# Kernel optimization log

Measured on AMD Instinct MI355X. Metric: run time of the kernel, lower is better.

The kernel has to match this reference:

```python
import jax, jax.numpy as jnp
import numpy as np

NUM_NODES = 102400
NUM_EDGES = 3276800
NUM_GRAPHS = 1024
LAMBDA_MAX = 2.0


def setup_inputs() -> dict:
    key = jax.random.key(0)
    ks = jax.random.split(key, 12)
    inp = {}
    inp['x'] = jax.random.normal(ks[0], (NUM_NODES, 128), dtype=jnp.float32)
    inp['edge_index'] = jax.random.randint(ks[1], (2, NUM_EDGES), 0, NUM_NODES, dtype=jnp.int32).astype(jnp.int64)
    inp['edge_attr'] = jax.random.uniform(ks[2], (NUM_EDGES,), dtype=jnp.float32)
    inp['batch'] = jnp.sort(jax.random.randint(ks[3], (NUM_NODES,), 0, NUM_GRAPHS, dtype=jnp.int32).astype(jnp.int64))
    inp['w1'] = jax.random.normal(ks[4], (3, 128, 64), dtype=jnp.float32) * 0.05
    inp['b1'] = jax.random.normal(ks[5], (64,), dtype=jnp.float32) * 0.05
    inp['w2'] = jax.random.normal(ks[6], (3, 64, 64), dtype=jnp.float32) * 0.05
    inp['b2'] = jax.random.normal(ks[7], (64,), dtype=jnp.float32) * 0.05
    inp['w3'] = jax.random.normal(ks[8], (3, 64, 128), dtype=jnp.float32) * 0.05
    inp['b3'] = jax.random.normal(ks[9], (128,), dtype=jnp.float32) * 0.05
    inp['lin_w'] = jax.random.normal(ks[10], (128, 2), dtype=jnp.float32) * 0.05
    inp['lin_b'] = jax.random.normal(ks[11], (2,), dtype=jnp.float32) * 0.05
    return inp


def _cheb_norm(edge_index, edge_attr, num_nodes):
    # PyG ChebConv.__norm__ with normalization='sym', lambda_max=2.0:
    #   L = I - D^{-1/2} A D^{-1/2};  Lhat = (2/lambda_max) * L - I
    # off-diagonal weights: -(2/lmax) * d_i^{-1/2} w_ij d_j^{-1/2}
    # diagonal coefficient:  (2/lmax) - 1  (== 0 for lmax = 2)
    src, dst = edge_index[0], edge_index[1]
    deg = jax.ops.segment_sum(edge_attr, src, num_segments=num_nodes)
    dinv = jnp.where(deg > 0, jax.lax.rsqrt(jnp.where(deg > 0, deg, 1.0)), 0.0)
    w = -(2.0 / LAMBDA_MAX) * dinv[src] * edge_attr * dinv[dst]
    diag = (2.0 / LAMBDA_MAX) - 1.0
    return w, diag


def _cheb_conv(x, src, dst, norm_w, diag, weight, bias):
    # weight: [K, Fin, Fout]; Chebyshev recurrence T0=x, T1=Lhat x, Tk=2 Lhat T_{k-1} - T_{k-2}
    n = x.shape[0]

    def spmv(v):  # Lhat @ v via edge-list scatter/gather
        return jax.ops.segment_sum(norm_w[:, None] * v[src], dst, num_segments=n) + diag * v

    Tx0 = x
    out = Tx0 @ weight[0]
    Tx1 = spmv(Tx0)
    out = out + Tx1 @ weight[1]
    for k in range(2, weight.shape[0]):
        Tx2 = 2.0 * spmv(Tx1) - Tx0
        out = out + Tx2 @ weight[k]
        Tx0, Tx1 = Tx1, Tx2
    return out + bias


def reference(x, edge_index, edge_attr, batch, w1, b1, w2, b2, w3, b3, lin_w, lin_b):
    n = x.shape[0]
    src, dst = edge_index[0], edge_index[1]
    norm_w, diag = _cheb_norm(edge_index, edge_attr, n)
    h = jax.nn.relu(_cheb_conv(x, src, dst, norm_w, diag, w1, b1))
    h = jax.nn.relu(_cheb_conv(h, src, dst, norm_w, diag, w2, b2))
    h = jax.nn.relu(_cheb_conv(h, src, dst, norm_w, diag, w3, b3))
    # global_mean_pool over graph ids
    sums = jax.ops.segment_sum(h, batch, num_segments=NUM_GRAPHS)
    cnts = jax.ops.segment_sum(jnp.ones((n,), h.dtype), batch, num_segments=NUM_GRAPHS)
    pooled = sums / jnp.maximum(cnts, 1.0)[:, None]
    return pooled @ lin_w + lin_b
```

## Files before the change

### kernel.cpp

```cpp
#include <hip/hip_runtime.h>
#include <cstddef>
#include <cstdint>

#define N_NODES 102400
#define N_EDGES 3276800
#define N_GRAPHS 1024
#define NBUCK 400
#define NBB 1024
#define EPB 3200
#define N64 ((size_t)N_NODES * 64)

typedef unsigned short ushortT;
typedef unsigned int uintT;
typedef __attribute__((ext_vector_type(8))) short bf16x8;
typedef __attribute__((ext_vector_type(4))) float f32x4;

__device__ __forceinline__ float b2f(ushortT h) {
    return __uint_as_float(((uintT)h) << 16);
}
__device__ __forceinline__ ushortT f2b(float f) {
    uintT u = __float_as_uint(f);
    uintT r = (u + 0x7fffu + ((u >> 16) & 1u)) >> 16;
    return (ushortT)r;
}
__device__ __forceinline__ float loF(uintT w) { return __uint_as_float(w << 16); }
__device__ __forceinline__ float hiF(uintT w) { return __uint_as_float(w & 0xffff0000u); }

__global__ __launch_bounds__(256) void k_binA(const int* __restrict__ src,
                                              const int* __restrict__ dst,
                                              int* __restrict__ blkCntD,
                                              int* __restrict__ blkCntS) {
    __shared__ int hd[NBUCK], hs[NBUCK];
    int t = threadIdx.x;
    for (int i = t; i < NBUCK; i += 256) { hd[i] = 0; hs[i] = 0; }
    __syncthreads();
    int base = blockIdx.x * EPB;
    const int4* s4 = (const int4*)(src + base);
    const int4* d4 = (const int4*)(dst + base);
    for (int v = t; v < EPB / 4; v += 256) {
        int4 d = d4[v];
        int4 s = s4[v];
        atomicAdd(&hd[d.x >> 8], 1);
        atomicAdd(&hd[d.y >> 8], 1);
        atomicAdd(&hd[d.z >> 8], 1);
        atomicAdd(&hd[d.w >> 8], 1);
        atomicAdd(&hs[s.x >> 8], 1);
        atomicAdd(&hs[s.y >> 8], 1);
        atomicAdd(&hs[s.z >> 8], 1);
        atomicAdd(&hs[s.w >> 8], 1);
    }
    __syncthreads();
    for (int i = t; i < NBUCK; i += 256) {
        blkCntD[(size_t)blockIdx.x * NBUCK + i] = hd[i];
        blkCntS[(size_t)blockIdx.x * NBUCK + i] = hs[i];
    }
}

__global__ void k_tr(const int* __restrict__ inD, const int* __restrict__ inS,
                     int* __restrict__ outD, int* __restrict__ outS) {
    __shared__ int tile[32][33];
    const int* in = blockIdx.z ? inS : inD;
    int* out = blockIdx.z ? outS : outD;
    int x = blockIdx.x * 32 + threadIdx.x;
    int yb = blockIdx.y * 32;
    for (int dy = threadIdx.y; dy < 32; dy += 8) {
        int y = yb + dy;
        tile[dy][threadIdx.x] = (x < NBUCK) ? in[(size_t)y * NBUCK + x] : 0;
    }
    __syncthreads();
    int xo = yb + threadIdx.x;
    for (int dy = threadIdx.y; dy < 32; dy += 8) {
        int bo = blockIdx.x * 32 + dy;
        if (bo < NBUCK) out[(size_t)bo * NBB + xo] = tile[threadIdx.x][dy];
    }
}

__global__ __launch_bounds__(512) void k_bbase(const int* __restrict__ blkCntT,
                                               int* __restrict__ blkRel,
                                               int* __restrict__ bucketTot) {
    __shared__ int sc[NBB];
    int b = blockIdx.x, t = threadIdx.x;
    int v0 = blkCntT[(size_t)b * NBB + t];
    int v1 = blkCntT[(size_t)b * NBB + t + 512];
    sc[t] = v0; sc[t + 512] = v1;
    __syncthreads();
    for (int o = 1; o < NBB; o <<= 1) {
        int x0 = (t >= o) ? sc[t - o] : 0;
        int x1 = (t + 512 >= o) ? sc[t + 512 - o] : 0;
        __syncthreads();
        sc[t] += x0; sc[t + 512] += x1;
        __syncthreads();
    }
    blkRel[(size_t)t * NBUCK + b] = sc[t] - v0;
    blkRel[(size_t)(t + 512) * NBUCK + b] = sc[t + 512] - v1;
    if (t == 511) bucketTot[b] = sc[NBB - 1];
}

__global__ __launch_bounds__(512) void k_bscan(const int* __restrict__ bucketTotD,
                                               const int* __restrict__ bucketTotS,
                                               int* __restrict__ binBaseD,
                                               int* __restrict__ binBaseS,
                                               int* __restrict__ rowp) {
    __shared__ int sc[512];
    int t = threadIdx.x;
    int vD = (t < NBUCK) ? bucketTotD[t] : 0;
    sc[t] = vD;
    __syncthreads();
    for (int o = 1; o < 512; o <<= 1) {
        int x = (t >= o) ? sc[t - o] : 0;
        __syncthreads();
        sc[t] += x;
        __syncthreads();
    }
    if (t < NBUCK) binBaseD[t] = sc[t] - vD;
    if (t == 511) { binBaseD[NBUCK] = sc[511]; rowp[N_NODES] = sc[511]; }
    __syncthreads();
    int vS = (t < NBUCK) ? bucketTotS[t] : 0;
    sc[t] = vS;
    __syncthreads();
    for (int o = 1; o < 512; o <<= 1) {
        int x = (t >= o) ? sc[t - o] : 0;
        __syncthreads();
        sc[t] += x;
        __syncthreads();
    }
    if (t < NBUCK) binBaseS[t] = sc[t] - vS;
    if (t == 511) binBaseS[NBUCK] = sc[511];
}

__global__ __launch_bounds__(512) void k_binB2(const int* __restrict__ src,
                                               const int* __restrict__ dst,
                                               const float* __restrict__ attr,
                                               const int* __restrict__ blkCntD,
                                               const int* __restrict__ blkCntS,
                                               const int* __restrict__ blkRelD,
                                               const int* __restrict__ blkRelS,
                                               const int* __restrict__ binBaseD,
                                               const int* __restrict__ binBaseS,
                                               int2* __restrict__ edsD,
                                               int2* __restrict__ edsS) {
    __shared__ int sxD[EPB];
    __shared__ int syD[EPB];
    __shared__ ushortT spD[EPB];
    __shared__ int sxS[EPB];
    __shared__ int syS[EPB];
    __shared__ ushortT spS[EPB];
    __shared__ int lcurD[NBUCK], deltaD[NBUCK];
    __shared__ int lcurS[NBUCK], deltaS[NBUCK];
    int bx = blockIdx.x, t = threadIdx.x;

    int vD = (t < NBUCK) ? blkCntD[(size_t)bx * NBUCK + t] : 0;
    int vS = (t < NBUCK) ? blkCntS[(size_t)bx * NBUCK + t] : 0;
    sxD[t] = vD; sxS[t] = vS;
    __syncthreads();
    for (int o = 1; o < 512; o <<= 1) {
        int xD = (t >= o) ? sxD[t - o] : 0;
        int xS = (t >= o) ? sxS[t - o] : 0;
        __syncthreads();
        sxD[t] += xD; sxS[t] += xS;
        __syncthreads();
    }
    if (t < NBUCK) {
        int eD = sxD[t] - vD;
        lcurD[t] = eD;
        deltaD[t] = binBaseD[t] + blkRelD[(size_t)bx * NBUCK + t] - eD;
        int eS = sxS[t] - vS;
        lcurS[t] = eS;
        deltaS[t] = binBaseS[t] + blkRelS[(size_t)bx * NBUCK + t] - eS;
    }
    __syncthreads();

    int base = bx * EPB;
    for (int v = t; v < EPB / 2; v += 512) {
        int e0 = base + v * 2;
        int2 s2 = *(const int2*)(src + e0);
        int2 d2 = *(const int2*)(dst + e0);
        float2 a2 = *(const float2*)(attr + e0);
        int bkt, lp;
        bkt = d2.x >> 8;
        lp = atomicAdd(&lcurD[bkt], 1);
        spD[lp] = (ushortT)bkt; sxD[lp] = (s2.x << 8) | (d2.x & 255);
        syD[lp] = __float_as_int(a2.x);
        bkt = s2.x >> 8;
        lp = atomicAdd(&lcurS[bkt], 1);
        spS[lp] = (ushortT)bkt; sxS[lp] = s2.x & 255;
        syS[lp] = __float_as_int(a2.x);
        bkt = d2.y >> 8;
        lp = atomicAdd(&lcurD[bkt], 1);
        spD[lp] = (ushortT)bkt; sxD[lp] = (s2.y << 8) | (d2.y & 255);
        syD[lp] = __float_as_int(a2.y);
        bkt = s2.y >> 8;
        lp = atomicAdd(&lcurS[bkt], 1);
        spS[lp] = (ushortT)bkt; sxS[lp] = s2.y & 255;
        syS[lp] = __float_as_int(a2.y);
    }
    __syncthreads();
    for (int i = t; i < EPB; i += 512) {
        edsD[i + deltaD[spD[i]]] = make_int2(sxD[i], syD[i]);
        edsS[i + deltaS[spS[i]]] = make_int2(sxS[i], syS[i]);
    }
}

__global__ __launch_bounds__(256) void k_deg(const int2* __restrict__ edsS,
                                             const int* __restrict__ binBaseS,
                                             float* __restrict__ dinv) {
    __shared__ float degL[256];
    int b = blockIdx.x, t = threadIdx.x;
    degL[t] = 0.f;
    __syncthreads();
    int s0 = binBaseS[b], s1 = binBaseS[b + 1];
    for (int i = s0 + t; i < s1; i += 256) {
        int2 e = edsS[i];
        atomicAdd(&degL[e.x], __int_as_float(e.y));
    }
    __syncthreads();
    float d = degL[t];
    dinv[b * 256 + t] = d > 0.f ? rsqrtf(d) : 0.f;
}

__global__ __launch_bounds__(512) void k_csr(const int2* __restrict__ edsD,
                                             const int* __restrict__ binBaseD,
                                             const float* __restrict__ dinvG,
                                             int* __restrict__ rowp,
                                             int2* __restrict__ cedge) {
    __shared__ int cntL[256];
    __shared__ int curL[256];
    __shared__ float dL[256];
    int b = blockIdx.x, t = threadIdx.x;
    if (t < 256) { cntL[t] = 0; dL[t] = dinvG[b * 256 + t]; }
    __syncthreads();
    int s0 = binBaseD[b], s1 = binBaseD[b + 1];
    for (int i = s0 + t; i < s1; i += 512) {
        atomicAdd(&cntL[edsD[i].x & 255], 1);
    }
    __syncthreads();
    int v = (t < 256) ? cntL[t] : 0;
    for (int o = 1; o < 256; o <<= 1) {
        int x = (t < 256 && t >= o) ? cntL[t - o] : 0;
        __syncthreads();
        if (t < 256) cntL[t] += x;
        __syncthreads();
    }
    if (t < 256) {
        int excl = cntL[t] - v;
        curL[t] = s0 + excl;
        rowp[b * 256 + t] = s0 + excl;
    }
    __syncthreads();
    for (int i = s0 + t; i < s1; i += 512) {
        int2 e = edsD[i];
        int dl = e.x & 255;
        int sg = e.x >> 8;
        float w = -__int_as_float(e.y) * dinvG[sg] * dL[dl];
        int p = atomicAdd(&curL[dl], 1);
        cedge[p] = make_int2(sg, __float_as_int(w));
    }
}

__global__ __launch_bounds__(256) void k_cast(const float* __restrict__ x,
                                              ushortT* __restrict__ Xhi,
                                              ushortT* __restrict__ Xlo) {
    int i = blockIdx.x * 256 + threadIdx.x;
    int n = i >> 5;
    int kq = (i & 31) * 4;
    float4 v = ((const float4*)x)[i];
    int s = kq >> 6, kk = kq & 63;
    size_t o = (size_t)s * N64 + (size_t)n * 64 + kk;
    ushort4 h, l;
    h.x = f2b(v.x); l.x = f2b(v.x - b2f(h.x));
    h.y = f2b(v.y); l.y = f2b(v.y - b2f(h.y));
    h.z = f2b(v.z); l.z = f2b(v.z - b2f(h.z));
    h.w = f2b(v.w); l.w = f2b(v.w - b2f(h.w));
    *(ushort4*)(Xhi + o) = h;
    *(ushort4*)(Xlo + o) = l;
}

__global__ void k_wprepAll(const float* __restrict__ w1f,
                           const float* __restrict__ w2f,
                           const float* __restrict__ w3f,
                           ushortT* __restrict__ Wt1h, ushortT* __restrict__ Wt1l,
                           ushortT* __restrict__ Wt2h, ushortT* __restrict__ Wt2l,
                           ushortT* __restrict__ Wt3h, ushortT* __restrict__ Wt3l) {
    int bid = blockIdx.x;
    float v;
    if (bid < 96) {
        int i = bid * 256 + threadIdx.x;
        int n = i / 128, k = i % 128;
        const float* w = w1f;
        if (n < 64)       v = w[k * 64 + n] - w[16384 + k * 64 + n];
        else if (n < 128) v = w[8192 + k * 64 + (n - 64)];
        else              v = w[16384 + k * 64 + (n - 128)];
        ushortT h = f2b(v);
        Wt1h[i] = h;
        Wt1l[i] = f2b(v - b2f(h));
    } else if (bid < 144) {
        int i = (bid - 96) * 256 + threadIdx.x;
        int n = i / 64, k = i % 64;
        const float* w = w2f;
        if (n < 64)       v = w[k * 64 + n] - w[8192 + k * 64 + n];
        else if (n < 128) v = w[4096 + k * 64 + (n - 64)];
        else              v = w[8192 + k * 64 + (n - 128)];
        ushortT h = f2b(v);
        Wt2h[i] = h;
        Wt2l[i] = f2b(v - b2f(h));
    } else {
        int i = (bid - 144) * 256 + threadIdx.x;
        int n = i / 192, k = i % 192;
        v = w3f[(k >> 6) * 8192 + (k & 63) * 128 + n];
        ushortT h = f2b(v);
        Wt3h[i] = h;
        Wt3l[i] = f2b(v - b2f(h));
    }
}

template <int KTOT, int NTOT, int MODE>
__global__ __launch_bounds__(512) void k_mgemm(
    const ushortT* __restrict__ Ah0, const ushortT* __restrict__ Ah1,
    const ushortT* __restrict__ Ah2, const ushortT* __restrict__ Al0,
    const ushortT* __restrict__ Al1, const ushortT* __restrict__ Al2,
    const ushortT* __restrict__ Wth, const ushortT* __restrict__ Wtl,
    const float* __restrict__ bias, float* __restrict__ outf,
    ushortT* __restrict__ outb, const int* __restrict__ batch,
    float* __restrict__ pooled, float* __restrict__ gcnt) {
    constexpr int KPAD = 72;
    constexpr int NCT = NTOT / 16;
    constexpr int SMEM_STAGE = 2 * NTOT * KPAD * 2;
    constexpr int SMEM_POOL = (MODE == 1) ? (256 * 128 * 4 + 256 * 4) : 0;
    constexpr int SMEM_BYTES = SMEM_STAGE > SMEM_POOL ? SMEM_STAGE : SMEM_POOL;
    __shared__ __align__(16) char smem[SMEM_BYTES];
    ushortT* Bh = (ushortT*)smem;
    ushortT* Bl = Bh + NTOT * KPAD;
    const ushortT* Ah[3] = {Ah0, Ah1, Ah2};
    const ushortT* Al[3] = {Al0, Al1, Al2};
    int t = threadIdx.x;
    int lane = t & 63;
    int wv = t >> 6;
    int m = lane & 15, q = lane >> 4;
    int r0 = blockIdx.x * 256 + wv * 32;
    int ar0 = r0 + m;
    int ar1 = r0 + 16 + m;

    f32x4 acc[2][NCT];
#pragma unroll
    for (int rf = 0; rf < 2; rf++)
#pragma unroll
        for (int ct = 0; ct < NCT; ct++)
#pragma unroll
            for (int j = 0; j < 4; j++) acc[rf][ct][j] = 0.f;

#pragma unroll
    for (int kc = 0; kc < KTOT / 64; kc++) {
        __syncthreads();
        for (int i = t; i < NTOT * 8; i += 512) {
            int col = i >> 3, k = (i & 7) * 8;
            *(uint4*)(Bh + col * KPAD + k) =
                *(const uint4*)(Wth + (size_t)col * KTOT + kc * 64 + k);
            *(uint4*)(Bl + col * KPAD + k) =
                *(const uint4*)(Wtl + (size_t)col * KTOT + kc * 64 + k);
        }
        __syncthreads();
        const ushortT* Ahc = Ah[kc];
        const ushortT* Alc = Al[kc];
#pragma unroll
        for (int ks2 = 0; ks2 < 2; ks2++) {
            int kk = ks2 * 32 + q * 8;
            bf16x8 ah0 = *(const bf16x8*)(Ahc + (size_t)ar0 * 64 + kk);
            bf16x8 al0 = *(const bf16x8*)(Alc + (size_t)ar0 * 64 + kk);
            bf16x8 ah1 = *(const bf16x8*)(Ahc + (size_t)ar1 * 64 + kk);
            bf16x8 al1 = *(const bf16x8*)(Alc + (size_t)ar1 * 64 + kk);
#pragma unroll
            for (int ct = 0; ct < NCT; ct++) {
                int bo = (ct * 16 + m) * KPAD + ks2 * 32 + q * 8;
                bf16x8 bh = *(const bf16x8*)(Bh + bo);
                bf16x8 bl = *(const bf16x8*)(Bl + bo);
                acc[0][ct] = __builtin_amdgcn_mfma_f32_16x16x32_bf16(ah0, bh, acc[0][ct], 0, 0, 0);
                acc[0][ct] = __builtin_amdgcn_mfma_f32_16x16x32_bf16(al0, bh, acc[0][ct], 0, 0, 0);
                acc[0][ct] = __builtin_amdgcn_mfma_f32_16x16x32_bf16(ah0, bl, acc[0][ct], 0, 0, 0);
                acc[1][ct] = __builtin_amdgcn_mfma_f32_16x16x32_bf16(ah1, bh, acc[1][ct], 0, 0, 0);
                acc[1][ct] = __builtin_amdgcn_mfma_f32_16x16x32_bf16(al1, bh, acc[1][ct], 0, 0, 0);
                acc[1][ct] = __builtin_amdgcn_mfma_f32_16x16x32_bf16(ah1, bl, acc[1][ct], 0, 0, 0);
            }
        }
    }

    if (MODE == 0) {
#pragma unroll
        for (int rf = 0; rf < 2; rf++)
#pragma unroll
            for (int ct = 0; ct < NCT; ct++)
#pragma unroll
                for (int rg = 0; rg < 4; rg++) {
                    int row = r0 + rf * 16 + q * 4 + rg;
                    float v = acc[rf][ct][rg];
                    if (ct < 8)
                        outf[(size_t)row * 128 + ct * 16 + m] = v;
                    else
                        outb[(size_t)row * 64 + (ct - 8) * 16 + m] = f2b(v);
                }
    } else {
        float* poolB = (float*)smem;
        int* batchL = (int*)(smem + 256 * 128 * 4);
        __syncthreads();
        for (int i = t; i < 256; i += 512)
            batchL[i] = batch[blockIdx.x * 256 + i];
#pragma unroll
        for (int rf = 0; rf < 2; rf++)
#pragma unroll
            for (int ct = 0; ct < NCT; ct++)
#pragma unroll
                for (int rg = 0; rg < 4; rg++) {
                    int rl = wv * 32 + rf * 16 + q * 4 + rg;
                    int col = ct * 16 + m;
                    poolB[rl * 128 + col] = fmaxf(acc[rf][ct][rg] + bias[col], 0.f);
                }
        __syncthreads();
        int col = t & 127, seg = t >> 7;
        int base = seg * 64;
        int g = batchL[base];
        float a = 0.f;
        int c = 0;
        for (int k = 0; k < 64; k++) {
            int gn = batchL[base + k];
            if (gn != g) {
                atomicAdd(&pooled[(size_t)g * 128 + col], a);
                if (col == 0) atomicAdd(&gcnt[g], (float)c);
                g = gn; a = 0.f; c = 0;
            }
            a += poolB[(base + k) * 128 + col];
            c++;
        }
        atomicAdd(&pooled[(size_t)g * 128 + col], a);
        if (col == 0) atomicAdd(&gcnt[g], (float)c);
    }
}

template <int MODE, int SA, bool AUXB, bool WLO>
__global__ __launch_bounds__(256) void k_spmm(const int* __restrict__ rowp,
                                              const int2* __restrict__ cedge,
                                              const ushortT* __restrict__ Xb,
                                              const float* __restrict__ auxF,
                                              const ushortT* __restrict__ auxH,
                                              const ushortT* __restrict__ auxL,
                                              const float* __restrict__ bias,
                                              ushortT* __restrict__ Yh,
                                              ushortT* __restrict__ Yl) {
    int node = blockIdx.x * 4 + (threadIdx.x >> 6);
    int lane = threadIdx.x & 63;
    int q = lane >> 3;
    int f = (lane & 7) * 8;
    int s = rowp[node], e = rowp[node + 1];
    const ushortT* Xf = Xb + f;
    float a0 = 0.f, a1 = 0.f, a2 = 0.f, a3 = 0.f;
    float a4 = 0.f, a5 = 0.f, a6 = 0.f, a7 = 0.f;
    for (int i = s; i < e; i += 16) {
        int i0 = min(i + q, e - 1);
        int i1 = min(i + 8 + q, e - 1);
        int2 ed0 = cedge[i0];
        int2 ed1 = cedge[i1];
        float w0 = (i + q < e) ? __int_as_float(ed0.y) : 0.f;
        float w1 = (i + 8 + q < e) ? __int_as_float(ed1.y) : 0.f;
        uint4 u0 = *(const uint4*)(Xf + ((size_t)ed0.x << 6));
        uint4 u1 = *(const uint4*)(Xf + ((size_t)ed1.x << 6));
        a0 = fmaf(w0, loF(u0.x), a0);
        a1 = fmaf(w0, hiF(u0.x), a1);
        a2 = fmaf(w0, loF(u0.y), a2);
        a3 = fmaf(w0, hiF(u0.y), a3);
        a4 = fmaf(w0, loF(u0.z), a4);
        a5 = fmaf(w0, hiF(u0.z), a5);
        a6 = fmaf(w0, loF(u0.w), a6);
        a7 = fmaf(w0, hiF(u0.w), a7);
        a0 = fmaf(w1, loF(u1.x), a0);
        a1 = fmaf(w1, hiF(u1.x), a1);
        a2 = fmaf(w1, loF(u1.y), a2);
        a3 = fmaf(w1, hiF(u1.y), a3);
        a4 = fmaf(w1, loF(u1.z), a4);
        a5 = fmaf(w1, hiF(u1.z), a5);
        a6 = fmaf(w1, loF(u1.w), a6);
        a7 = fmaf(w1, hiF(u1.w), a7);
    }
    a0 += __shfl_xor(a0, 8); a0 += __shfl_xor(a0, 16); a0 += __shfl_xor(a0, 32);
    a1 += __shfl_xor(a1, 8); a1 += __shfl_xor(a1, 16); a1 += __shfl_xor(a1, 32);
    a2 += __shfl_xor(a2, 8); a2 += __shfl_xor(a2, 16); a2 += __shfl_xor(a2, 32);
    a3 += __shfl_xor(a3, 8); a3 += __shfl_xor(a3, 16); a3 += __shfl_xor(a3, 32);
    a4 += __shfl_xor(a4, 8); a4 += __shfl_xor(a4, 16); a4 += __shfl_xor(a4, 32);
    a5 += __shfl_xor(a5, 8); a5 += __shfl_xor(a5, 16); a5 += __shfl_xor(a5, 32);
    a6 += __shfl_xor(a6, 8); a6 += __shfl_xor(a6, 16); a6 += __shfl_xor(a6, 32);
    a7 += __shfl_xor(a7, 8); a7 += __shfl_xor(a7, 16); a7 += __shfl_xor(a7, 32);

    if (q == 0 || (WLO && q == 1)) {
        float x0 = 0.f, x1 = 0.f, x2 = 0.f, x3 = 0.f;
        float x4 = 0.f, x5 = 0.f, x6 = 0.f, x7 = 0.f;
        if (MODE != 0) {
            if (AUXB) {
                uint4 ha = *(const uint4*)(auxH + (size_t)node * 64 + f);
                uint4 la = *(const uint4*)(auxL + (size_t)node * 64 + f);
                x0 = loF(ha.x) + loF(la.x);
                x1 = hiF(ha.x) + hiF(la.x);
                x2 = loF(ha.y) + loF(la.y);
                x3 = hiF(ha.y) + hiF(la.y);
                x4 = loF(ha.z) + loF(la.z);
                x5 = hiF(ha.z) + hiF(la.z);
                x6 = loF(ha.w) + loF(la.w);
                x7 = hiF(ha.w) + hiF(la.w);
            } else {
                float4 av0 = *(const float4*)(auxF + (size_t)node * SA + f);
                float4 av1 = *(const float4*)(auxF + (size_t)node * SA + f + 4);
                x0 = av0.x; x1 = av0.y; x2 = av0.z; x3 = av0.w;
                x4 = av1.x; x5 = av1.y; x6 = av1.z; x7 = av1.w;
            }
        }
        float r0, r1, r2, r3, r4, r5, r6, r7;
        if (MODE == 0) {
            r0 = a0; r1 = a1; r2 = a2; r3 = a3;
            r4 = a4; r5 = a5; r6 = a6; r7 = a7;
        } else if (MODE == 1) {
            r0 = x0 + 2.f * a0; r1 = x1 + 2.f * a1;
            r2 = x2 + 2.f * a2; r3 = x3 + 2.f * a3;
            r4 = x4 + 2.f * a4; r5 = x5 + 2.f * a5;
            r6 = x6 + 2.f * a6; r7 = x7 + 2.f * a7;
        } else if (MODE == 2) {
            r0 = 2.f * a0 - x0; r1 = 2.f * a1 - x1;
            r2 = 2.f * a2 - x2; r3 = 2.f * a3 - x3;
            r4 = 2.f * a4 - x4; r5 = 2.f * a5 - x5;
            r6 = 2.f * a6 - x6; r7 = 2.f * a7 - x7;
        } else {
            float4 bv0 = *(const float4*)(bias + f);
            float4 bv1 = *(const float4*)(bias + f + 4);
            r0 = fmaxf(x0 + a0 + bv0.x, 0.f);
            r1 = fmaxf(x1 + a1 + bv0.y, 0.f);
            r2 = fmaxf(x2 + a2 + bv0.z, 0.f);
            r3 = fmaxf(x3 + a3 + bv0.w, 0.f);
            r4 = fmaxf(x4 + a4 + bv1.x, 0.f);
            r5 = fmaxf(x5 + a5 + bv1.y, 0.f);
            r6 = fmaxf(x6 + a6 + bv1.z, 0.f);
            r7 = fmaxf(x7 + a7 + bv1.w, 0.f);
        }
        ushortT h0 = f2b(r0), h1 = f2b(r1), h2 = f2b(r2), h3 = f2b(r3);
        ushortT h4 = f2b(r4), h5 = f2b(r5), h6 = f2b(r6), h7 = f2b(r7);
        if (q == 0) {
            uint4 pk;
            pk.x = (uintT)h0 | ((uintT)h1 << 16);
            pk.y = (uintT)h2 | ((uintT)h3 << 16);
            pk.z = (uintT)h4 | ((uintT)h5 << 16);
            pk.w = (uintT)h6 | ((uintT)h7 << 16);
            *(uint4*)(Yh + (size_t)node * 64 + f) = pk;
        } else {
            uint4 pk;
            pk.x = (uintT)f2b(r0 - b2f(h0)) | ((uintT)f2b(r1 - b2f(h1)) << 16);
            pk.y = (uintT)f2b(r2 - b2f(h2)) | ((uintT)f2b(r3 - b2f(h3)) << 16);
            pk.z = (uintT)f2b(r4 - b2f(h4)) | ((uintT)f2b(r5 - b2f(h5)) << 16);
            pk.w = (uintT)f2b(r6 - b2f(h6)) | ((uintT)f2b(r7 - b2f(h7)) << 16);
            *(uint4*)(Yl + (size_t)node * 64 + f) = pk;
        }
    }
}

__global__ void k_final(const float* __restrict__ pooled, const float* __restrict__ gcnt,
                        const float* __restrict__ lin_w, const float* __restrict__ lin_b,
                        float* __restrict__ out) {
    int g = blockIdx.x * 4 + (threadIdx.x >> 6);
    int lane = threadIdx.x & 63;
    if (g >= N_GRAPHS) return;
    float inv = 1.f / fmaxf(gcnt[g], 1.f);
    float v0 = pooled[(size_t)g * 128 + lane] * inv;
    float v1 = pooled[(size_t)g * 128 + 64 + lane] * inv;
    float p0 = v0 * lin_w[lane * 2 + 0] + v1 * lin_w[(lane + 64) * 2 + 0];
    float p1 = v0 * lin_w[lane * 2 + 1] + v1 * lin_w[(lane + 64) * 2 + 1];
    for (int o = 32; o > 0; o >>= 1) {
        p0 += __shfl_down(p0, o);
        p1 += __shfl_down(p1, o);
    }
    if (lane == 0) {
        out[g * 2 + 0] = p0 + lin_b[0];
        out[g * 2 + 1] = p1 + lin_b[1];
    }
}

extern "C" void kernel_launch(void* const* d_in, const int* in_sizes, int n_in,
                              void* d_out, int out_size, void* d_ws, size_t ws_size,
                              hipStream_t stream) {
    const float* x     = (const float*)d_in[0];
    const int*   src   = (const int*)d_in[1];
    const int*   dst   = src + N_EDGES;
    const float* eattr = (const float*)d_in[2];
    const int*   batch = (const int*)d_in[3];
    const float* w1    = (const float*)d_in[4];
    const float* b1    = (const float*)d_in[5];
    const float* w2    = (const float*)d_in[6];
    const float* b2    = (const float*)d_in[7];
    const float* w3    = (const float*)d_in[8];
    const float* b3    = (const float*)d_in[9];
    const float* lin_w = (const float*)d_in[10];
    const float* lin_b = (const float*)d_in[11];
    float* out = (float*)d_out;

    char* ws = (char*)d_ws;
    size_t off = 0;
    auto alloc = [&](size_t bytes) -> char* {
        char* p = ws + off;
        off += (bytes + 255) & ~(size_t)255;
        return p;
    };
    int*   blkCntD   = (int*)  alloc((size_t)NBB * NBUCK * 4);
    int*   blkCntS   = (int*)  alloc((size_t)NBB * NBUCK * 4);
    int*   blkCntDT  = (int*)  alloc((size_t)NBUCK * NBB * 4);
    int*   blkCntST  = (int*)  alloc((size_t)NBUCK * NBB * 4);
    int*   blkRelD   = (int*)  alloc((size_t)NBB * NBUCK * 4);
    int*   blkRelS   = (int*)  alloc((size_t)NBB * NBUCK * 4);
    int*   bucketTotD = (int*) alloc(NBUCK * 4);
    int*   bucketTotS = (int*) alloc(NBUCK * 4);
    int*   binBaseD  = (int*)  alloc((NBUCK + 1) * 4);
    int*   binBaseS  = (int*)  alloc((NBUCK + 1) * 4);
    float* dinv      = (float*)alloc((size_t)N_NODES * 4);
    int*   rowp      = (int*)  alloc((size_t)(N_NODES + 1) * 4);
    ushortT* Wt1h   = (ushortT*)alloc(192 * 128 * 2);
    ushortT* Wt1l   = (ushortT*)alloc(192 * 128 * 2);
    ushortT* Wt2h   = (ushortT*)alloc(192 * 64 * 2);
    ushortT* Wt2l   = (ushortT*)alloc(192 * 64 * 2);
    ushortT* Wt3h   = (ushortT*)alloc(128 * 192 * 2);
    ushortT* Wt3l   = (ushortT*)alloc(128 * 192 * 2);
    float* pooled   = (float*)alloc((size_t)(N_GRAPHS * 128 + N_GRAPHS) * 4);
    float* gcnt     = pooled + (size_t)N_GRAPHS * 128;
    int2*  cedge    = (int2*) alloc((size_t)N_EDGES * 8);
    char*  Buf1     = alloc((size_t)N_EDGES * 16);
    char*  Buf2     = alloc((size_t)N_NODES * 128 * 4);
    char*  Buf3     = alloc(4 * N64 * 2);

    int2* edsD = (int2*)Buf1;
    int2* edsS = edsD + N_EDGES;
    ushortT* Xhi  = (ushortT*)Buf1;
    ushortT* Xlo  = Xhi + 2 * N64;
    ushortT* GThi = (ushortT*)Buf1;
    float* P  = (float*)Buf2;
    ushortT* G0    = (ushortT*)Buf3;
    ushortT* Qhi   = G0 + N64;
    ushortT* H1hi  = G0 + 2 * N64;
    ushortT* H1lo  = G0 + 3 * N64;
    ushortT* GTlo0 = G0;
    ushortT* GTlo1 = H1hi;
    ushortT* GTlo2 = H1lo;

    hipMemsetAsync(pooled, 0, (size_t)(N_GRAPHS * 128 + N_GRAPHS) * 4, stream);

    k_binA<<<NBB, 256, 0, stream>>>(src, dst, blkCntD, blkCntS);
    k_tr<<<dim3(13, 32, 2), dim3(32, 8), 0, stream>>>(blkCntD, blkCntS,
                                                      blkCntDT, blkCntST);
    k_bbase<<<NBUCK, 512, 0, stream>>>(blkCntDT, blkRelD, bucketTotD);
    k_bbase<<<NBUCK, 512, 0, stream>>>(blkCntST, blkRelS, bucketTotS);
    k_bscan<<<1, 512, 0, stream>>>(bucketTotD, bucketTotS, binBaseD, binBaseS, rowp);
    k_binB2<<<NBB, 512, 0, stream>>>(src, dst, eattr, blkCntD, blkCntS,
                                     blkRelD, blkRelS, binBaseD, binBaseS,
                                     edsD, edsS);
    k_deg<<<NBUCK, 256, 0, stream>>>(edsS, binBaseS, dinv);
    k_csr<<<NBUCK, 512, 0, stream>>>(edsD, binBaseD, dinv, rowp, cedge);

    k_cast<<<N_NODES * 32 / 256, 256, 0, stream>>>(x, Xhi, Xlo);
    k_wprepAll<<<240, 256, 0, stream>>>(w1, w2, w3, Wt1h, Wt1l, Wt2h, Wt2l,
                                        Wt3h, Wt3l);

    k_mgemm<128, 192, 0><<<N_NODES / 256, 512, 0, stream>>>(
        Xhi, Xhi + N64, nullptr, Xlo, Xlo + N64, nullptr, Wt1h, Wt1l, nullptr,
        P, G0, nullptr, nullptr, nullptr);
    k_spmm<1, 128, false, false><<<N_NODES / 4, 256, 0, stream>>>(
        rowp, cedge, G0, P + 64, nullptr, nullptr, nullptr, Qhi, nullptr);
    k_spmm<3, 128, false, true><<<N_NODES / 4, 256, 0, stream>>>(
        rowp, cedge, Qhi, P, nullptr, nullptr, b1, H1hi, H1lo);

    k_mgemm<64, 192, 0><<<N_NODES / 256, 512, 0, stream>>>(
        H1hi, nullptr, nullptr, H1lo, nullptr, nullptr, Wt2h, Wt2l, nullptr,
        P, G0, nullptr, nullptr, nullptr);
    k_spmm<1, 128, false, false><<<N_NODES / 4, 256, 0, stream>>>(
        rowp, cedge, G0, P + 64, nullptr, nullptr, nullptr, Qhi, nullptr);
    k_spmm<3, 128, false, true><<<N_NODES / 4, 256, 0, stream>>>(
        rowp, cedge, Qhi, P, nullptr, nullptr, b2, GThi, GTlo0);

    k_spmm<0, 64, false, true><<<N_NODES / 4, 256, 0, stream>>>(
        rowp, cedge, GThi, nullptr, nullptr, nullptr, nullptr, GThi + N64, GTlo1);
    k_spmm<2, 64, true, true><<<N_NODES / 4, 256, 0, stream>>>(
        rowp, cedge, GThi + N64, nullptr, GThi, GTlo0, nullptr, GThi + 2 * N64, GTlo2);
    k_mgemm<192, 128, 1><<<N_NODES / 256, 512, 0, stream>>>(
        GThi, GThi + N64, GThi + 2 * N64, GTlo0, GTlo1, GTlo2, Wt3h, Wt3l, b3,
        nullptr, nullptr, batch, pooled, gcnt);

    k_final<<<N_GRAPHS / 4, 256, 0, stream>>>(pooled, gcnt, lin_w, lin_b, out);
}
```

Before: 715.0 us.

## Halve binning block size and shrink GEMM LDS stage to 32-wide K chunks

The edge binning now uses 2048 blocks of 1600 edges instead of 1024 blocks of 3200. This shrinks per-block shared memory and spreads the work over more blocks, so the block-base scan now has each thread prefix four entries serially. The MFMA GEMM stages the weight tile in 32-wide K chunks with a smaller padded LDS buffer, cutting LDS use to allow more resident blocks. The cost is twice as many barrier-separated weight loads, and more count and offset arrays to scan.

```diff
diff --git a/kernel.cpp b/kernel.cpp
--- a/kernel.cpp
+++ b/kernel.cpp
@@ -6,8 +6,8 @@
 #define N_EDGES 3276800
 #define N_GRAPHS 1024
 #define NBUCK 400
-#define NBB 1024
-#define EPB 3200
+#define NBB 2048
+#define EPB 1600
 #define N64 ((size_t)N_NODES * 64)
 
 typedef unsigned short ushortT;
@@ -78,22 +78,30 @@
 __global__ __launch_bounds__(512) void k_bbase(const int* __restrict__ blkCntT,
                                                int* __restrict__ blkRel,
                                                int* __restrict__ bucketTot) {
-    __shared__ int sc[NBB];
+    __shared__ int sc[512];
     int b = blockIdx.x, t = threadIdx.x;
-    int v0 = blkCntT[(size_t)b * NBB + t];
-    int v1 = blkCntT[(size_t)b * NBB + t + 512];
-    sc[t] = v0; sc[t + 512] = v1;
-    __syncthreads();
-    for (int o = 1; o < NBB; o <<= 1) {
-        int x0 = (t >= o) ? sc[t - o] : 0;
-        int x1 = (t + 512 >= o) ? sc[t + 512 - o] : 0;
-        __syncthreads();
-        sc[t] += x0; sc[t + 512] += x1;
-        __syncthreads();
-    }
-    blkRel[(size_t)t * NBUCK + b] = sc[t] - v0;
-    blkRel[(size_t)(t + 512) * NBUCK + b] = sc[t + 512] - v1;
-    if (t == 511) bucketTot[b] = sc[NBB - 1];
+    int v[4];
+    int loc = 0;
+#pragma unroll
+    for (int j = 0; j < 4; j++) {
+        v[j] = blkCntT[(size_t)b * NBB + t * 4 + j];
+        loc += v[j];
+    }
+    sc[t] = loc;
+    __syncthreads();
+    for (int o = 1; o < 512; o <<= 1) {
+        int x = (t >= o) ? sc[t - o] : 0;
+        __syncthreads();
+        sc[t] += x;
+        __syncthreads();
+    }
+    int run = sc[t] - loc;
+#pragma unroll
+    for (int j = 0; j < 4; j++) {
+        blkRel[(size_t)(t * 4 + j) * NBUCK + b] = run;
+        run += v[j];
+    }
+    if (t == 511) bucketTot[b] = run;
 }
 
 __global__ __launch_bounds__(512) void k_bscan(const int* __restrict__ bucketTotD,
@@ -171,28 +179,20 @@
     __syncthreads();
 
     int base = bx * EPB;
-    for (int v = t; v < EPB / 2; v += 512) {
-        int e0 = base + v * 2;
-        int2 s2 = *(const int2*)(src + e0);
-        int2 d2 = *(const int2*)(dst + e0);
-        float2 a2 = *(const float2*)(attr + e0);
+    for (int v = t; v < EPB; v += 512) {
+        int e0 = base + v;
+        int s0 = src[e0];
+        int d0 = dst[e0];
+        float a0 = attr[e0];
         int bkt, lp;
-        bkt = d2.x >> 8;
+        bkt = d0 >> 8;
         lp = atomicAdd(&lcurD[bkt], 1);
-        spD[lp] = (ushortT)bkt; sxD[lp] = (s2.x << 8) | (d2.x & 255);
-        syD[lp] = __float_as_int(a2.x);
-        bkt = s2.x >> 8;
+        spD[lp] = (ushortT)bkt; sxD[lp] = (s0 << 8) | (d0 & 255);
+        syD[lp] = __float_as_int(a0);
+        bkt = s0 >> 8;
         lp = atomicAdd(&lcurS[bkt], 1);
-        spS[lp] = (ushortT)bkt; sxS[lp] = s2.x & 255;
-        syS[lp] = __float_as_int(a2.x);
-        bkt = d2.y >> 8;
-        lp = atomicAdd(&lcurD[bkt], 1);
-        spD[lp] = (ushortT)bkt; sxD[lp] = (s2.y << 8) | (d2.y & 255);
-        syD[lp] = __float_as_int(a2.y);
-        bkt = s2.y >> 8;
-        lp = atomicAdd(&lcurS[bkt], 1);
-        spS[lp] = (ushortT)bkt; sxS[lp] = s2.y & 255;
-        syS[lp] = __float_as_int(a2.y);
+        spS[lp] = (ushortT)bkt; sxS[lp] = s0 & 255;
+        syS[lp] = __float_as_int(a0);
     }
     __syncthreads();
     for (int i = t; i < EPB; i += 512) {
@@ -322,7 +322,7 @@
     const float* __restrict__ bias, float* __restrict__ outf,
     ushortT* __restrict__ outb, const int* __restrict__ batch,
     float* __restrict__ pooled, float* __restrict__ gcnt) {
-    constexpr int KPAD = 72;
+    constexpr int KPAD = 40;
     constexpr int NCT = NTOT / 16;
     constexpr int SMEM_STAGE = 2 * NTOT * KPAD * 2;
     constexpr int SMEM_POOL = (MODE == 1) ? (256 * 128 * 4 + 256 * 4) : 0;
@@ -349,37 +349,36 @@
             for (int j = 0; j < 4; j++) acc[rf][ct][j] = 0.f;
 
 #pragma unroll
-    for (int kc = 0; kc < KTOT / 64; kc++) {
-        __syncthreads();
-        for (int i = t; i < NTOT * 8; i += 512) {
-            int col = i >> 3, k = (i & 7) * 8;
+    for (int kc = 0; kc < KTOT / 32; kc++) {
+        __syncthreads();
+        for (int i = t; i < NTOT * 4; i += 512) {
+            int col = i >> 2, k = (i & 3) * 8;
             *(uint4*)(Bh + col * KPAD + k) =
-                *(const uint4*)(Wth + (size_t)col * KTOT + kc * 64 + k);
+                *(const uint4*)(Wth + (size_t)col * KTOT + kc * 32 + k);
             *(uint4*)(Bl + col * KPAD + k) =
-                *(const uint4*)(Wtl + (size_t)col * KTOT + kc * 64 + k);
+                *(const uint4*)(Wtl + (size_t)col * KTOT + kc * 32 + k);
         }
         __syncthreads();
-        const ushortT* Ahc = Ah[kc];
-        const ushortT* Alc = Al[kc];
-#pragma unroll
-        for (int ks2 = 0; ks2 < 2; ks2++) {
-            int kk = ks2 * 32 + q * 8;
-            bf16x8 ah0 = *(const bf16x8*)(Ahc + (size_t)ar0 * 64 + kk);
-            bf16x8 al0 = *(const bf16x8*)(Alc + (size_t)ar0 * 64 + kk);
-            bf16x8 ah1 = *(const bf16x8*)(Ahc + (size_t)ar1 * 64 + kk);
-            bf16x8 al1 = *(const bf16x8*)(Alc + (size_t)ar1 * 64 + kk);
-#pragma unroll
-            for (int ct = 0; ct < NCT; ct++) {
-                int bo = (ct * 16 + m) * KPAD + ks2 * 32 + q * 8;
-                bf16x8 bh = *(const bf16x8*)(Bh + bo);
-                bf16x8 bl = *(const bf16x8*)(Bl + bo);
-                acc[0][ct] = __builtin_amdgcn_mfma_f32_16x16x32_bf16(ah0, bh, acc[0][ct], 0, 0, 0);
-                acc[0][ct] = __builtin_amdgcn_mfma_f32_16x16x32_bf16(al0, bh, acc[0][ct], 0, 0, 0);
-                acc[0][ct] = __builtin_amdgcn_mfma_f32_16x16x32_bf16(ah0, bl, acc[0][ct], 0, 0, 0);
-                acc[1][ct] = __builtin_amdgcn_mfma_f32_16x16x32_bf16(ah1, bh, acc[1][ct], 0, 0, 0);
-                acc[1][ct] = __builtin_amdgcn_mfma_f32_16x16x32_bf16(al1, bh, acc[1][ct], 0, 0, 0);
-                acc[1][ct] = __builtin_amdgcn_mfma_f32_16x16x32_bf16(ah1, bl, acc[1][ct], 0, 0, 0);
-            }
+        int k0 = kc * 32;
+        int slot = k0 >> 6;
+        int kk = (k0 & 63) + q * 8;
+        const ushortT* Ahc = Ah[slot];
+        const ushortT* Alc = Al[slot];
+        bf16x8 ah0 = *(const bf16x8*)(Ahc + (size_t)ar0 * 64 + kk);
+        bf16x8 al0 = *(const bf16x8*)(Alc + (size_t)ar0 * 64 + kk);
+        bf16x8 ah1 = *(const bf16x8*)(Ahc + (size_t)ar1 * 64 + kk);
+        bf16x8 al1 = *(const bf16x8*)(Alc + (size_t)ar1 * 64 + kk);
+#pragma unroll
+        for (int ct = 0; ct < NCT; ct++) {
+            int bo = (ct * 16 + m) * KPAD + q * 8;
+            bf16x8 bh = *(const bf16x8*)(Bh + bo);
+            bf16x8 bl = *(const bf16x8*)(Bl + bo);
+            acc[0][ct] = __builtin_amdgcn_mfma_f32_16x16x32_bf16(ah0, bh, acc[0][ct], 0, 0, 0);
+            acc[0][ct] = __builtin_amdgcn_mfma_f32_16x16x32_bf16(al0, bh, acc[0][ct], 0, 0, 0);
+            acc[0][ct] = __builtin_amdgcn_mfma_f32_16x16x32_bf16(ah0, bl, acc[0][ct], 0, 0, 0);
+            acc[1][ct] = __builtin_amdgcn_mfma_f32_16x16x32_bf16(ah1, bh, acc[1][ct], 0, 0, 0);
+            acc[1][ct] = __builtin_amdgcn_mfma_f32_16x16x32_bf16(al1, bh, acc[1][ct], 0, 0, 0);
+            acc[1][ct] = __builtin_amdgcn_mfma_f32_16x16x32_bf16(ah1, bl, acc[1][ct], 0, 0, 0);
         }
     }
 
@@ -643,8 +642,8 @@
     hipMemsetAsync(pooled, 0, (size_t)(N_GRAPHS * 128 + N_GRAPHS) * 4, stream);
 
     k_binA<<<NBB, 256, 0, stream>>>(src, dst, blkCntD, blkCntS);
-    k_tr<<<dim3(13, 32, 2), dim3(32, 8), 0, stream>>>(blkCntD, blkCntS,
-                                                      blkCntDT, blkCntST);
+    k_tr<<<dim3(13, NBB / 32, 2), dim3(32, 8), 0, stream>>>(blkCntD, blkCntS,
+                                                            blkCntDT, blkCntST);
     k_bbase<<<NBUCK, 512, 0, stream>>>(blkCntDT, blkRelD, bucketTotD);
     k_bbase<<<NBUCK, 512, 0, stream>>>(blkCntST, blkRelS, bucketTotS);
     k_bscan<<<1, 512, 0, stream>>>(bucketTotD, bucketTotS, binBaseD, binBaseS, rowp);
```

Result: slower. 735.7 us (+2.9%).
